# Kernel optimization log

Hardware: AMD Instinct MI355X
Metric: run time of the kernel (lower is better)

Reference implementation:

```python
import jax, jax.numpy as jnp
import numpy as np

K = 9
HF = WF = 128
SAMPLING = 16
H_IMG = W_IMG = 2048.0
ANC_RATIO = np.array([0.5, 1.0, 2.0])
ANC_SIZE = np.array([8.0, 16.0, 32.0])
TOPN_NMS = 6000
N_NMS = 2000
THR_NMS = 0.7


def generate_anchors():
    # loop order in original GenerateAnchor: ii over Wf (ctrx), jj over Hf (ctry), ratio, size
    ctrx = (np.arange(WF) + 0.5) * SAMPLING  # [Wf]
    ctry = (np.arange(HF) + 0.5) * SAMPLING  # [Hf]
    w = SAMPLING * ANC_SIZE[None, :] / np.sqrt(ANC_RATIO)[:, None]  # [R,S]
    h = SAMPLING * ANC_SIZE[None, :] * np.sqrt(ANC_RATIO)[:, None]
    cx = ctrx[:, None, None, None]  # [Wf,1,1,1]
    cy = ctry[None, :, None, None]  # [1,Hf,1,1]
    w = w[None, None]; h = h[None, None]  # [1,1,R,S]
    x1, y1 = cx - w / 2, cy - h / 2
    x2, y2 = cx + w / 2, cy + h / 2
    anc = np.stack(np.broadcast_arrays(x1, y1, x2, y2), axis=-1).reshape(-1, 4)
    return np.round(anc).astype(np.float32)  # [Wf*Hf*K, 4]


def conv2d(x, w, b, pad):
    y = jax.lax.conv_general_dilated(
        x, w, (1, 1), [(pad, pad), (pad, pad)],
        dimension_numbers=('NCHW', 'OIHW', 'NCHW'))
    return y + b[None, :, None, None]


def pairwise_iou(b):
    # Faithful to my_IoU: 'gt' (pivot, row i) coords are int-truncated;
    # intersection via min(all)+w_a+w_g-max(all); union uses raw/truncated areas.
    ax1, ay1, ax2, ay2 = b[:, 0], b[:, 1], b[:, 2], b[:, 3]
    aw, ah = ax2 - ax1, ay2 - ay1
    aminx, amaxx = jnp.minimum(ax1, ax2), jnp.maximum(ax1, ax2)
    aminy, amaxy = jnp.minimum(ay1, ay2), jnp.maximum(ay1, ay2)
    tx1, ty1, tx2, ty2 = jnp.trunc(ax1), jnp.trunc(ay1), jnp.trunc(ax2), jnp.trunc(ay2)
    gminx, gmaxx = jnp.minimum(tx1, tx2), jnp.maximum(tx1, tx2)
    gminy, gmaxy = jnp.minimum(ty1, ty2), jnp.maximum(ty1, ty2)
    gw, gh = jnp.trunc(ax2 - ax1), jnp.trunc(ay2 - ay1)
    iw = jnp.maximum(jnp.minimum(aminx[None, :], gminx[:, None]) + aw[None, :]
                     + gw[:, None] - jnp.maximum(amaxx[None, :], gmaxx[:, None]), 0.0)
    ih = jnp.maximum(jnp.minimum(aminy[None, :], gminy[:, None]) + ah[None, :]
                     + gh[:, None] - jnp.maximum(amaxy[None, :], gmaxy[:, None]), 0.0)
    inter = iw * ih  # [i=pivot, j=candidate]
    union = (aw * ah)[None, :] + (gw * gh)[:, None] - inter
    return inter / union


def make_roi(anchor, delta, obj):
    # delta2xy
    aw = anchor[:, 2] - anchor[:, 0]
    ah = anchor[:, 3] - anchor[:, 1]
    acx = anchor[:, 0] + aw / 2
    acy = anchor[:, 1] + ah / 2
    cx = delta[:, 0] * aw + acx
    cy = delta[:, 1] * ah + acy
    w = jnp.exp(delta[:, 2]) * aw
    h = jnp.exp(delta[:, 3]) * ah
    roi = jnp.stack([cx - w / 2, cy - h / 2, cx + w / 2, cy + h / 2], axis=1)
    # clip exactly as original: negatives->0; >H -> H-1; >W -> W-1
    roi = jnp.maximum(roi, 0.0)
    roi = roi.at[:, 3].set(jnp.where(roi[:, 3] > H_IMG, H_IMG - 1.0, roi[:, 3]))
    roi = roi.at[:, 2].set(jnp.where(roi[:, 2] > W_IMG, W_IMG - 1.0, roi[:, 2]))
    valid = (roi[:, 2] - roi[:, 0] > SAMPLING) & (roi[:, 3] - roi[:, 1] > SAMPLING)
    scores = jnp.where(valid, obj, -jnp.inf)  # mask instead of dropping (jit-friendly)
    top_scores, top_idx = jax.lax.top_k(scores, TOPN_NMS)
    boxes = roi[top_idx]
    keep0 = jnp.isfinite(top_scores)
    iou = pairwise_iou(boxes)  # [TOPN, TOPN]
    idxs = jnp.arange(TOPN_NMS)

    def body(i, keep):
        sup = keep[i] & (iou[i] >= THR_NMS) & (idxs > i)
        return keep & ~sup

    keep = jax.lax.fori_loop(0, TOPN_NMS, body, keep0)
    rank = jnp.cumsum(keep) - 1
    pos = jnp.where(keep & (rank < N_NMS), rank, N_NMS)  # out-of-range rows dropped
    out = jnp.zeros((N_NMS, 4), boxes.dtype).at[pos].set(boxes, mode='drop')
    return out


def setup_inputs() -> dict:
    key = jax.random.key(0)
    ks = jax.random.split(key, 4)
    featmap = jax.random.normal(ks[0], (1, 512, HF, WF), dtype=jnp.float32)
    conv3_w = jax.random.normal(ks[1], (512, 512, 3, 3), dtype=jnp.float32) * 0.01
    conv3_b = jnp.zeros((512,), jnp.float32)
    cls_w = jax.random.normal(ks[2], (2 * K, 512, 1, 1), dtype=jnp.float32) * 0.01
    cls_b = jnp.zeros((2 * K,), jnp.float32)
    reg_w = jax.random.normal(ks[3], (4 * K, 512, 1, 1), dtype=jnp.float32) * 0.01
    reg_b = jnp.zeros((4 * K,), jnp.float32)
    return {'featmap': featmap, 'conv3_w': conv3_w, 'conv3_b': conv3_b,
            'cls_w': cls_w, 'cls_b': cls_b, 'reg_w': reg_w, 'reg_b': reg_b}


def reference(featmap, conv3_w, conv3_b, cls_w, cls_b, reg_w, reg_b):
    x = jax.nn.relu(conv2d(featmap, conv3_w, conv3_b, 1))
    pred_cls = conv2d(x, cls_w, cls_b, 0)  # [1, 2k, Hf, Wf]
    pred_reg = conv2d(x, reg_w, reg_b, 0)  # [1, 4k, Hf, Wf]
    pred_cls = jnp.transpose(pred_cls, (0, 2, 3, 1)).reshape(1, -1, 2)
    pred_reg = jnp.transpose(pred_reg, (0, 2, 3, 1)).reshape(1, -1, 4)
    pred_obj = pred_cls[:, :, 1]
    anchors = jnp.asarray(generate_anchors())
    # roi path is detached in the original (uses .data)
    roi = make_roi(anchors,
                   jax.lax.stop_gradient(pred_reg[0]),
                   jax.lax.stop_gradient(pred_obj[0]))
    return roi, pred_cls, pred_reg
```

## Files before the change

kernel.cpp:

```cpp
#include <hip/hip_runtime.h>

#define HF 128
#define WF 128
#define KANC 9
#define NANC (HF*WF*KANC)
#define NSORT 262144
#define TOPN 6000
#define NWORDS 94
#define NOUT 2000
#define OFF_CLS 8000
#define OFF_REG 302912
#define NCAND 8192
#define NBCAP 2048

typedef unsigned long long u64;
typedef double d4 __attribute__((ext_vector_type(4)));
typedef const __attribute__((address_space(1))) void* gas1;
typedef __attribute__((address_space(3))) void* las3;

__global__ __launch_bounds__(256) void zero2_k(double* p1, int n1,
                                               double* p2, int n2) {
  int i = blockIdx.x * 256 + threadIdx.x;
  if (i < n1) p1[i] = 0.0;
  else if (i - n1 < n2) p2[i - n1] = 0.0;
}

__global__ __launch_bounds__(256) void wtrans_k(const float* __restrict__ w,
                                                float* __restrict__ wt) {
  __shared__ float ld[64 * 73];
  int t = threadIdx.x;
  int ocg = blockIdx.x & 7, icg = blockIdx.x >> 3;
  int oc0 = ocg << 6, ic0 = icg << 3;
  #pragma unroll
  for (int rep = 0; rep < 18; ++rep) {
    int idx = rep * 256 + t;
    int row = idx / 72, col = idx - row * 72;
    ld[row * 73 + col] = w[(size_t)(oc0 + row) * 4608 + ic0 * 9 + col];
  }
  __syncthreads();
  #pragma unroll
  for (int rep = 0; rep < 18; ++rep) {
    int idx = rep * 256 + t;
    int pair = idx >> 6, oc = idx & 63;
    int tap = pair % 9, ic = pair / 9;
    wt[(size_t)tap * 262144 + (size_t)(ic0 + ic) * 512 + oc0 + oc] =
        ld[oc * 73 + ic * 9 + tap];
  }
}

#define BKC 32
#define NCHUNK 144

__global__ __launch_bounds__(256, 3) void conv_mfma_k(
    const float* __restrict__ feat, const float* __restrict__ wt,
    const float* __restrict__ conv_b, const float* __restrict__ cls_w,
    const float* __restrict__ reg_w, double* __restrict__ predacc)
{
  __shared__ __align__(16) char smraw[49152];
  float* AsB = (float*)smraw;
  float* BsB = (float*)(smraw + 2 * 32 * 64 * 4);
  int tid = threadIdx.x;
  int bid = blockIdx.x;
  int pt = bid & 255, ot = bid >> 8;
  int h = pt >> 1, w0 = (pt & 1) << 6;
  int oc0 = ot << 7;
  int wv = tid >> 6, l = tid & 63;
  int wr = wv >> 1, wc = wv & 1;
  int lg = l >> 4, lr = l & 15;

  d4 acc[2][4];
  #pragma unroll
  for (int t = 0; t < 2; ++t)
    #pragma unroll
    for (int u = 0; u < 4; ++u) acc[t][u] = (d4)0.0;

  float4 areg[2];

  auto gloadA = [&](int c) {
    int tap = c >> 4, ic0 = (c & 15) << 5;
    int kh = tap / 3 - 1, kw = tap % 3 - 1;
    int hp = h + kh;
    bool okh = ((unsigned)hp < 128u);
    #pragma unroll
    for (int i = 0; i < 2; ++i) {
      int q = tid + (i << 8);
      int r = q >> 4, c0 = (q & 15) << 2;
      float v0 = 0.f, v1 = 0.f, v2 = 0.f, v3 = 0.f;
      const float* src = &feat[((ic0 + r) << 14) + (hp << 7)];
      int wp = w0 + c0 + kw;
      if (okh) {
        if ((unsigned)(wp + 0) < 128u) v0 = src[wp + 0];
        if ((unsigned)(wp + 1) < 128u) v1 = src[wp + 1];
        if ((unsigned)(wp + 2) < 128u) v2 = src[wp + 2];
        if ((unsigned)(wp + 3) < 128u) v3 = src[wp + 3];
      }
      areg[i] = make_float4(v0, v1, v2, v3);
    }
  };
  auto gloadB_lds = [&](int c, int buf) {
    float* B = BsB + buf * (32 * 128);
    #pragma unroll
    for (int i = 0; i < 4; ++i) {
      int q = tid + (i << 8);
      int r = q >> 5, c0 = (q & 31) << 2;
      const float* src =
          &wt[(size_t)((c << 5) + r) * 512 + oc0 + (c0 ^ ((r & 1) << 4))];
      __builtin_amdgcn_global_load_lds((gas1)src, (las3)&B[q << 2], 16, 0, 0);
    }
  };
  auto dswriteA = [&](int buf) {
    float* A = AsB + buf * (32 * 64);
    #pragma unroll
    for (int i = 0; i < 2; ++i) {
      int q = tid + (i << 8);
      int r = q >> 4, c0 = (q & 15) << 2;
      *(float4*)&A[(r << 6) + (c0 ^ ((r & 1) << 4))] = areg[i];
    }
  };
  auto compute = [&](int buf) {
    const float* A = AsB + buf * (32 * 64);
    const float* B = BsB + buf * (32 * 128);
    #pragma unroll
    for (int k4 = 0; k4 < BKC; k4 += 4) {
      int krow = k4 + lg;
      int sw = (krow & 1) << 4;
      double a0 = (double)A[(krow << 6) + (((wr << 5) + lr) ^ sw)];
      double a1 = (double)A[(krow << 6) + (((wr << 5) + 16 + lr) ^ sw)];
      double b0 = (double)B[(krow << 7) + (((wc << 6) + lr) ^ sw)];
      double b1 = (double)B[(krow << 7) + (((wc << 6) + 16 + lr) ^ sw)];
      double b2 = (double)B[(krow << 7) + (((wc << 6) + 32 + lr) ^ sw)];
      double b3 = (double)B[(krow << 7) + (((wc << 6) + 48 + lr) ^ sw)];
      acc[0][0] = __builtin_amdgcn_mfma_f64_16x16x4f64(a0, b0, acc[0][0], 0, 0, 0);
      acc[0][1] = __builtin_amdgcn_mfma_f64_16x16x4f64(a0, b1, acc[0][1], 0, 0, 0);
      acc[0][2] = __builtin_amdgcn_mfma_f64_16x16x4f64(a0, b2, acc[0][2], 0, 0, 0);
      acc[0][3] = __builtin_amdgcn_mfma_f64_16x16x4f64(a0, b3, acc[0][3], 0, 0, 0);
      acc[1][0] = __builtin_amdgcn_mfma_f64_16x16x4f64(a1, b0, acc[1][0], 0, 0, 0);
      acc[1][1] = __builtin_amdgcn_mfma_f64_16x16x4f64(a1, b1, acc[1][1], 0, 0, 0);
      acc[1][2] = __builtin_amdgcn_mfma_f64_16x16x4f64(a1, b2, acc[1][2], 0, 0, 0);
      acc[1][3] = __builtin_amdgcn_mfma_f64_16x16x4f64(a1, b3, acc[1][3], 0, 0, 0);
    }
  };

  gloadA(0);
  gloadB_lds(0, 0);
  dswriteA(0);
  for (int c = 0; c < NCHUNK; ++c) {
    __syncthreads();
    if (c + 1 < NCHUNK) {
      gloadB_lds(c + 1, (c + 1) & 1);
      gloadA(c + 1);
    }
    compute(c & 1);
    if (c + 1 < NCHUNK) dswriteA((c + 1) & 1);
  }

  int rmap[4], cmap[4];
  {
    d4 z = (d4)0.0;
    double apr = (lg == 0) ? (double)lr : 0.0;
    double bpr = (lg == 0) ? 1.0 : 0.0;
    d4 dr = __builtin_amdgcn_mfma_f64_16x16x4f64(apr, bpr, z, 0, 0, 0);
    double apc = (lg == 0) ? 1.0 : 0.0;
    double bpc = (lg == 0) ? (double)lr : 0.0;
    d4 dc = __builtin_amdgcn_mfma_f64_16x16x4f64(apc, bpc, z, 0, 0, 0);
    #pragma unroll
    for (int r = 0; r < 4; ++r) { rmap[r] = (int)dr[r]; cmap[r] = (int)dc[r]; }
  }

  double* xs = (double*)smraw;
  float* hwS = (float*)(smraw + 64 * 65 * 8);
  double sacc[14];
  #pragma unroll
  for (int it = 0; it < 14; ++it) sacc[it] = 0.0;

  #pragma unroll
  for (int hh = 0; hh < 2; ++hh) {
    __syncthreads();
    for (int e = tid; e < 54 * 64; e += 256) {
      int o = e >> 6, j = e & 63;
      int oc = oc0 + (hh << 6) + j;
      hwS[e] = (o < 18) ? cls_w[(o << 9) + oc] : reg_w[((o - 18) << 9) + oc];
    }
    if (wc == hh) {
      #pragma unroll
      for (int t = 0; t < 2; ++t) {
        #pragma unroll
        for (int u = 0; u < 4; ++u) {
          #pragma unroll
          for (int r = 0; r < 4; ++r) {
            int ocl = (u << 4) + cmap[r];
            int pxl = (wr << 5) + (t << 4) + rmap[r];
            double v = acc[t][u][r] + (double)conv_b[oc0 + (hh << 6) + ocl];
            xs[pxl * 65 + ocl] = (v > 0.0) ? v : 0.0;
          }
        }
      }
    }
    __syncthreads();
    #pragma unroll
    for (int it = 0; it < 14; ++it) {
      int e = tid + (it << 8);
      if (e < 54 * 64) {
        int o = e >> 6, px = e & 63;
        const double* xr = &xs[px * 65];
        const float* hr = &hwS[o << 6];
        double s = 0.0;
        #pragma unroll
        for (int j = 0; j < 64; ++j) s += xr[j] * (double)hr[j];
        sacc[it] += s;
      }
    }
  }
  int pixbase = (h << 7) + w0;
  #pragma unroll
  for (int it = 0; it < 14; ++it) {
    int e = tid + (it << 8);
    if (e < 54 * 64) {
      int o = e >> 6, px = e & 63;
      atomicAdd(&predacc[(size_t)(pixbase + px) * 54 + o], sacc[it]);
    }
  }
}

__global__ __launch_bounds__(256) void chk_x_k(
    const float* __restrict__ feat, const float* __restrict__ c3w,
    double* __restrict__ xraw)
{
  int task = blockIdx.x * 256 + threadIdx.x;
  int pi = task >> 12;
  int oc = (task >> 3) & 511;
  int icg = task & 7;
  const int pixs[4] = {0, 5437, 10240, 16383};
  int pix = pixs[pi];
  int h = pix >> 7, w = pix & 127;
  double s = 0.0;
  for (int ic = icg * 64; ic < icg * 64 + 64; ++ic) {
    const float* f = &feat[ic << 14];
    const float* wp = &c3w[(size_t)(oc * 512 + ic) * 9];
    #pragma unroll
    for (int kh = -1; kh <= 1; ++kh) {
      int hp = h + kh;
      if ((unsigned)hp >= 128u) continue;
      #pragma unroll
      for (int kw = -1; kw <= 1; ++kw) {
        int wq = w + kw;
        if ((unsigned)wq >= 128u) continue;
        s += (double)f[(hp << 7) + wq] * (double)wp[(kh + 1) * 3 + (kw + 1)];
      }
    }
  }
  atomicAdd(&xraw[(pi << 9) + oc], s);
}

__global__ __launch_bounds__(256) void chk_cmp_k(
    const double* __restrict__ xraw, const float* __restrict__ c3b,
    const float* __restrict__ cls_w, const float* __restrict__ reg_w,
    const double* __restrict__ predacc, double* flagd)
{
  int t = threadIdx.x;
  if (t >= 216) return;
  int pi = t / 54, o = t - pi * 54;
  const int pixs[4] = {0, 5437, 10240, 16383};
  const float* wrow = (o < 18) ? &cls_w[o << 9] : &reg_w[(o - 18) << 9];
  const double* xr = &xraw[pi << 9];
  double s = 0.0;
  for (int j = 0; j < 512; ++j) {
    double x = xr[j] + (double)c3b[j];
    x = x > 0.0 ? x : 0.0;
    s += x * (double)wrow[j];
  }
  double got = predacc[(size_t)pixs[pi] * 54 + o];
  if (fabs(got - s) > 1e-6) *flagd = 1.0;
}

__global__ __launch_bounds__(256) void rezero_k(const double* __restrict__ flagd,
                                                double* p, int n) {
  if (*flagd == 0.0) return;
  int i = blockIdx.x * 256 + threadIdx.x;
  if (i < n) p[i] = 0.0;
}

__global__ __launch_bounds__(256) void conv_fb_k(
    const double* __restrict__ flagd,
    const float* __restrict__ feat, const float* __restrict__ wt,
    const float* __restrict__ conv_b, const float* __restrict__ cls_w,
    const float* __restrict__ reg_w, double* __restrict__ predacc)
{
  if (*flagd == 0.0) return;
  __shared__ __align__(16) char smraw[47104];
  double* As = (double*)smraw;
  double* Bs = As + 2048;
  int tid = threadIdx.x;
  int bid = blockIdx.x;
  int pt = bid & 255, ot = bid >> 8;
  int h = pt >> 1, w0 = (pt & 1) << 6;
  int oc0 = ot << 6;
  int tx = tid & 15, ty = tid >> 4;

  double acc[4][4];
  #pragma unroll
  for (int i = 0; i < 4; ++i)
    #pragma unroll
    for (int j = 0; j < 4; ++j) acc[i][j] = 0.0;

  for (int tap = 0; tap < 9; ++tap) {
    int kh = tap / 3 - 1, kw = tap % 3 - 1;
    int hp = h + kh;
    bool okh = (hp >= 0) && (hp < HF);
    for (int icc = 0; icc < 16; ++icc) {
      int ic0 = icc << 5;
      __syncthreads();
      #pragma unroll
      for (int i = 0; i < 8; ++i) {
        int e = tid + (i << 8);
        int icl = e >> 6;
        int lx = e & 63;
        int wp = w0 + lx + kw;
        float v = 0.0f;
        if (okh && wp >= 0 && wp < WF)
          v = feat[((ic0 + icl) << 14) + (hp << 7) + wp];
        As[(icl << 6) + lx] = (double)v;
        Bs[(icl << 6) + lx] =
            (double)wt[((((tap << 9) + ic0 + icl)) << 9) + oc0 + lx];
      }
      __syncthreads();
      #pragma unroll
      for (int k = 0; k < 32; ++k) {
        const double* ar = &As[(k << 6) + (ty << 2)];
        const double* br = &Bs[(k << 6) + (tx << 2)];
        double a0 = ar[0], a1 = ar[1], a2 = ar[2], a3 = ar[3];
        double b0 = br[0], b1 = br[1], b2 = br[2], b3 = br[3];
        acc[0][0] += a0 * b0; acc[0][1] += a0 * b1; acc[0][2] += a0 * b2; acc[0][3] += a0 * b3;
        acc[1][0] += a1 * b0; acc[1][1] += a1 * b1; acc[1][2] += a1 * b2; acc[1][3] += a1 * b3;
        acc[2][0] += a2 * b0; acc[2][1] += a2 * b1; acc[2][2] += a2 * b2; acc[2][3] += a2 * b3;
        acc[3][0] += a3 * b0; acc[3][1] += a3 * b1; acc[3][2] += a3 * b2; acc[3][3] += a3 * b3;
      }
    }
  }
  __syncthreads();
  double* xs = (double*)smraw;
  float* hwS = (float*)(smraw + 64 * 65 * 8);
  #pragma unroll
  for (int i = 0; i < 4; ++i) {
    int px = (ty << 2) + i;
    #pragma unroll
    for (int j = 0; j < 4; ++j) {
      int oc = (tx << 2) + j;
      double v = acc[i][j] + (double)conv_b[oc0 + oc];
      xs[px * 65 + oc] = v > 0.0 ? v : 0.0;
    }
  }
  for (int e = tid; e < 54 * 64; e += 256) {
    int o = e >> 6, ocl = e & 63;
    hwS[e] = (o < 18) ? cls_w[(o << 9) + oc0 + ocl]
                      : reg_w[((o - 18) << 9) + oc0 + ocl];
  }
  __syncthreads();
  int pixbase = (h << 7) + w0;
  for (int e = tid; e < 54 * 64; e += 256) {
    int px = e & 63, o = e >> 6;
    const double* xr = &xs[px * 65];
    const float* hr = &hwS[o << 6];
    double s = 0.0;
    #pragma unroll
    for (int j = 0; j < 64; ++j) s += xr[j] * (double)hr[j];
    atomicAdd(&predacc[(pixbase + px) * 54 + o], s);
  }
}

__global__ __launch_bounds__(256) void anchor_k(
    const double* __restrict__ predacc, const float* __restrict__ cls_b,
    const float* __restrict__ reg_b, float* __restrict__ out,
    double* __restrict__ roi_all, double* __restrict__ scores_d,
    ulonglong2* __restrict__ sortb)
{
  #pragma clang fp contract(off)
  int a = blockIdx.x * 256 + threadIdx.x;
  if (a >= NSORT) return;
  if (a >= NANC) {
    sortb[a] = make_ulonglong2(0xFFF0000000000000ULL, 0xFFFFFFFFULL);
    return;
  }
  int pix = a / 9;
  int k = a - pix * 9;
  int h = pix >> 7, wq = pix & 127;
  const double* pa = &predacc[pix * 54];
  double c0 = pa[2 * k] + (double)cls_b[2 * k];
  double c1 = pa[2 * k + 1] + (double)cls_b[2 * k + 1];
  double d0 = pa[18 + 4 * k + 0] + (double)reg_b[4 * k + 0];
  double d1 = pa[18 + 4 * k + 1] + (double)reg_b[4 * k + 1];
  double d2 = pa[18 + 4 * k + 2] + (double)reg_b[4 * k + 2];
  double d3 = pa[18 + 4 * k + 3] + (double)reg_b[4 * k + 3];
  out[OFF_CLS + a * 2 + 0] = (float)c0;
  out[OFF_CLS + a * 2 + 1] = (float)c1;
  out[OFF_REG + a * 4 + 0] = (float)d0;
  out[OFF_REG + a * 4 + 1] = (float)d1;
  out[OFF_REG + a * 4 + 2] = (float)d2;
  out[OFF_REG + a * 4 + 3] = (float)d3;
  int ir = k / 3, is = k - ir * 3;
  double ratio = (ir == 0) ? 0.5 : (ir == 1 ? 1.0 : 2.0);
  double asz = (is == 0) ? 8.0 : (is == 1 ? 16.0 : 32.0);
  double sq = sqrt(ratio);
  double wa = (16.0 * asz) / sq;
  double ha = (16.0 * asz) * sq;
  double cx = (h + 0.5) * 16.0;
  double cy = (wq + 0.5) * 16.0;
  double A0 = (double)(float)rint(cx - wa * 0.5);
  double A1 = (double)(float)rint(cy - ha * 0.5);
  double A2 = (double)(float)rint(cx + wa * 0.5);
  double A3 = (double)(float)rint(cy + ha * 0.5);
  double aw = A2 - A0, ah = A3 - A1;
  double acx = A0 + aw * 0.5, acy = A1 + ah * 0.5;
  double ccx = d0 * aw + acx;
  double ccy = d1 * ah + acy;
  double wr = exp(d2) * aw;
  double hh = exp(d3) * ah;
  double r0 = ccx - wr * 0.5;
  double r1 = ccy - hh * 0.5;
  double r2 = ccx + wr * 0.5;
  double r3 = ccy + hh * 0.5;
  r0 = fmax(r0, 0.0); r1 = fmax(r1, 0.0); r2 = fmax(r2, 0.0); r3 = fmax(r3, 0.0);
  r3 = (r3 > 2048.0) ? 2047.0 : r3;
  r2 = (r2 > 2048.0) ? 2047.0 : r2;
  bool valid = ((r2 - r0) > 16.0) && ((r3 - r1) > 16.0);
  double score = valid ? c1 : -__builtin_huge_val();
  roi_all[a * 4 + 0] = r0;
  roi_all[a * 4 + 1] = r1;
  roi_all[a * 4 + 2] = r2;
  roi_all[a * 4 + 3] = r3;
  scores_d[a] = score;
  u64 u = (u64)__double_as_longlong(score);
  u64 m = (u >> 63) ? ~u : (u | 0x8000000000000000ULL);
  sortb[a] = make_ulonglong2(~m, (u64)a);
}

__global__ __launch_bounds__(1024) void init_sel_k(unsigned* hist, u64* selp,
                                                   unsigned* cnt) {
  int t = blockIdx.x * 1024 + threadIdx.x;
  if (t < 2048) hist[t] = 0;
  if (t == 0) { selp[0] = 0; selp[1] = 0; cnt[0] = 0; cnt[1] = 0; }
}

__global__ __launch_bounds__(1024) void hist_k(const ulonglong2* __restrict__ sortb,
                                               unsigned* __restrict__ hist,
                                               const u64* __restrict__ selp,
                                               int pass) {
  __shared__ unsigned h[2048];
  int t = threadIdx.x;
  h[t] = 0; h[t + 1024] = 0;
  __syncthreads();
  const int SH[3] = {53, 42, 31};
  const u64 PM[3] = {0ULL, 0xFFE0000000000000ULL, 0xFFFFFC0000000000ULL};
  u64 pfx = selp[0];
  u64 pm = PM[pass];
  int sh = SH[pass];
  for (int e = blockIdx.x * 1024 + t; e < NSORT; e += gridDim.x * 1024) {
    u64 k = sortb[e].x;
    if ((k & pm) == pfx)
      atomicAdd(&h[(unsigned)((k >> sh) & 2047)], 1u);
  }
  __syncthreads();
  if (h[t]) atomicAdd(&hist[t], h[t]);
  if (h[t + 1024]) atomicAdd(&hist[t + 1024], h[t + 1024]);
}

__global__ __launch_bounds__(1024) void scan_k(unsigned* hist, u64* selp, int pass) {
  __shared__ unsigned h[2048];
  int t = threadIdx.x;
  h[t] = hist[t]; h[t + 1024] = hist[t + 1024];
  hist[t] = 0; hist[t + 1024] = 0;
  __syncthreads();
  if (t == 0) {
    const int SH[3] = {53, 42, 31};
    u64 cum = selp[1];
    u64 pfx = selp[0];
    int b = 0;
    for (; b < 2047; ++b) {
      if (cum + h[b] >= (u64)TOPN) break;
      cum += h[b];
    }
    selp[0] = pfx | ((u64)b << SH[pass]);
    selp[1] = cum;
  }
}

__global__ __launch_bounds__(1024) void compact_k(
    const ulonglong2* __restrict__ sortb, const u64* __restrict__ selp,
    ulonglong2* __restrict__ cand, ulonglong2* __restrict__ bcand,
    unsigned* __restrict__ cnt) {
  u64 pfx = selp[0];
  const u64 M33 = 0xFFFFFFFF80000000ULL;
  for (int e = blockIdx.x * 1024 + threadIdx.x; e < NSORT; e += gridDim.x * 1024) {
    ulonglong2 v = sortb[e];
    u64 top = v.x & M33;
    if (top < pfx) {
      unsigned p = atomicAdd(&cnt[0], 1u);
      if (p < NCAND) cand[p] = v;
    } else if (top == pfx) {
      unsigned p = atomicAdd(&cnt[1], 1u);
      if (p < NBCAP) bcand[p] = v;
    }
  }
}

__global__ __launch_bounds__(1024) void fill_k(ulonglong2* cand,
                                               const ulonglong2* __restrict__ bcand,
                                               const unsigned* __restrict__ cnt) {
  int t = blockIdx.x * 1024 + threadIdx.x;
  unsigned ci = cnt[0];
  unsigned cb = cnt[1] < NBCAP ? cnt[1] : NBCAP;
  if (t >= (int)ci) {
    if (t < (int)(ci + cb)) cand[t] = bcand[t - ci];
    else if (t < NCAND) cand[t] = make_ulonglong2(~0ULL, ~0ULL);
  }
}

__device__ __forceinline__ bool sless(ulonglong2 A, ulonglong2 B) {
  return (A.x < B.x) || (A.x == B.x && A.y < B.y);
}

__global__ __launch_bounds__(1024) void sort8k_k(ulonglong2* d) {
  extern __shared__ ulonglong2 s[];
  int t = threadIdx.x;
  #pragma unroll
  for (int i = 0; i < 8; ++i) s[t + (i << 10)] = d[t + (i << 10)];
  __syncthreads();
  for (int k = 2; k <= NCAND; k <<= 1) {
    for (int j = k >> 1; j >= 1; j >>= 1) {
      #pragma unroll
      for (int q = 0; q < 4; ++q) {
        int p = t + (q << 10);
        int li = ((p & ~(j - 1)) << 1) | (p & (j - 1));
        int pa = li | j;
        bool asc = ((li & k) == 0);
        ulonglong2 A = s[li], B = s[pa];
        bool sw = asc ? sless(B, A) : sless(A, B);
        if (sw) { s[li] = B; s[pa] = A; }
      }
      __syncthreads();
    }
  }
  #pragma unroll
  for (int i = 0; i < 8; ++i) d[t + (i << 10)] = s[t + (i << 10)];
}

__global__ __launch_bounds__(1024) void prep_k(
    const ulonglong2* __restrict__ sorted, const double* __restrict__ roi_all,
    const double* __restrict__ scores_d, double* __restrict__ boxes,
    u64* __restrict__ removed)
{
  int t = threadIdx.x;
  for (int i = t; i < TOPN; i += 1024) {
    unsigned idx = (unsigned)sorted[i].y;
    double b0 = 0, b1 = 0, b2 = 0, b3 = 0;
    if (idx < NANC) {
      b0 = roi_all[idx * 4 + 0];
      b1 = roi_all[idx * 4 + 1];
      b2 = roi_all[idx * 4 + 2];
      b3 = roi_all[idx * 4 + 3];
    }
    boxes[i * 4 + 0] = b0; boxes[i * 4 + 1] = b1;
    boxes[i * 4 + 2] = b2; boxes[i * 4 + 3] = b3;
  }
  if (t < NWORDS) {
    u64 wdd = (t == NWORDS - 1) ? 0xFFFF000000000000ULL : 0ULL;
    for (int b = 0; b < 64; ++b) {
      int i = t * 64 + b;
      if (i >= TOPN) break;
      unsigned idx = (unsigned)sorted[i].y;
      bool dead = true;
      if (idx < NANC) dead = isinf(scores_d[idx]);
      if (dead) wdd |= (1ULL << b);
    }
    removed[t] = wdd;
  }
}

__global__ __launch_bounds__(256) void mask_k(const double* __restrict__ boxes,
                                              u64* __restrict__ mask) {
  #pragma clang fp contract(off)
  int gw = (blockIdx.x * 256 + threadIdx.x) >> 6;
  int lane = threadIdx.x & 63;
  int i = gw / NWORDS, wj = gw - i * NWORDS;
  if (i >= TOPN) return;
  if (wj < (i >> 6)) return;
  double ix1 = boxes[i * 4 + 0], iy1 = boxes[i * 4 + 1];
  double ix2 = boxes[i * 4 + 2], iy2 = boxes[i * 4 + 3];
  double tx1 = trunc(ix1), ty1 = trunc(iy1), tx2 = trunc(ix2), ty2 = trunc(iy2);
  double gminx = fmin(tx1, tx2), gmaxx = fmax(tx1, tx2);
  double gminy = fmin(ty1, ty2), gmaxy = fmax(ty1, ty2);
  double gw_ = trunc(ix2 - ix1), gh_ = trunc(iy2 - iy1);
  int j = wj * 64 + lane;
  bool pred = false;
  if (j < TOPN && j > i) {
    double jx1 = boxes[j * 4 + 0], jy1 = boxes[j * 4 + 1];
    double jx2 = boxes[j * 4 + 2], jy2 = boxes[j * 4 + 3];
    double aw = jx2 - jx1, ah = jy2 - jy1;
    double aminx = fmin(jx1, jx2), amaxx = fmax(jx1, jx2);
    double aminy = fmin(jy1, jy2), amaxy = fmax(jy1, jy2);
    double iw = fmin(aminx, gminx) + aw + gw_ - fmax(amaxx, gmaxx);
    iw = fmax(iw, 0.0);
    double ih = fmin(aminy, gminy) + ah + gh_ - fmax(amaxy, gmaxy);
    ih = fmax(ih, 0.0);
    double inter = iw * ih;
    double uni = aw * ah + gw_ * gh_ - inter;
    pred = (inter / uni >= 0.7);
  }
  u64 bal = __ballot(pred);
  if (lane == 0) mask[(size_t)i * NWORDS + wj] = bal;
}

__global__ __launch_bounds__(1024) void nms_chunk_k(const u64* __restrict__ mask,
                                                    u64* removed_g) {
  __shared__ u64 rem[NWORDS];
  __shared__ u64 aliveSh;
  int t = threadIdx.x;
  int lane = t & 63;
  int wvid = t >> 6;
  if (t < NWORDS) rem[t] = removed_g[t];
  __syncthreads();
  for (int c = 0; c < NWORDS; ++c) {
    if (wvid == 0) {
      int i = c * 64 + lane;
      u64 diag = (i < TOPN) ? mask[(size_t)i * NWORDS + c] : 0ULL;
      u64 local = rem[c];
      #pragma unroll 1
      for (int j = 0; j < 64; ++j) {
        u64 dj = __shfl(diag, j);
        if (!((local >> j) & 1ULL)) local |= dj;
      }
      if (lane == 0) { rem[c] = local; aliveSh = ~local; }
    }
    __syncthreads();
    u64 alive = aliveSh;
    int nw = NWORDS - 1 - c;
    if (nw > 0 && alive) {
      int npairs = 64 * nw;
      for (int p = t; p < npairs; p += 1024) {
        int j = p / nw;
        int w = c + 1 + (p - j * nw);
        if ((alive >> j) & 1ULL) {
          int i = c * 64 + j;
          if (i < TOPN) {
            u64 v = mask[(size_t)i * NWORDS + w];
            if (v) atomicOr(&rem[w], v);
          }
        }
      }
    }
    __syncthreads();
  }
  if (t < NWORDS) removed_g[t] = rem[t];
}

__global__ __launch_bounds__(256) void out_k(const u64* __restrict__ removed,
                                             const double* __restrict__ boxes,
                                             float* __restrict__ out) {
  __shared__ int pref[NWORDS + 1];
  __shared__ u64 keepw[NWORDS];
  int t = threadIdx.x;
  for (int i = t; i < NOUT * 4; i += 256) out[i] = 0.0f;
  if (t < NWORDS) keepw[t] = ~removed[t];
  __syncthreads();
  if (t == 0) {
    int s = 0;
    for (int w = 0; w < NWORDS; ++w) { pref[w] = s; s += __popcll(keepw[w]); }
    pref[NWORDS] = s;
  }
  __syncthreads();
  for (int i = t; i < TOPN; i += 256) {
    u64 kw = keepw[i >> 6];
    if ((kw >> (i & 63)) & 1ULL) {
      int rank = pref[i >> 6] + __popcll(kw & ((1ULL << (i & 63)) - 1ULL));
      if (rank < NOUT) {
        out[rank * 4 + 0] = (float)boxes[i * 4 + 0];
        out[rank * 4 + 1] = (float)boxes[i * 4 + 1];
        out[rank * 4 + 2] = (float)boxes[i * 4 + 2];
        out[rank * 4 + 3] = (float)boxes[i * 4 + 3];
      }
    }
  }
}

extern "C" void kernel_launch(void* const* d_in, const int* in_sizes, int n_in,
                              void* d_out, int out_size, void* d_ws, size_t ws_size,
                              hipStream_t stream) {
  const float* feat = (const float*)d_in[0];
  const float* c3w = (const float*)d_in[1];
  const float* c3b = (const float*)d_in[2];
  const float* clw = (const float*)d_in[3];
  const float* clb = (const float*)d_in[4];
  const float* rgw = (const float*)d_in[5];
  const float* rgb = (const float*)d_in[6];
  float* out = (float*)d_out;
  char* ws = (char*)d_ws;
  size_t off = 0;
  auto alloc = [&](size_t bytes) {
    size_t o = off;
    off = (off + bytes + 255) & ~(size_t)255;
    return o;
  };
  double* predacc = (double*)(ws + alloc(16384ULL * 54 * 8));
  double* flagd = (double*)(ws + alloc(256));
  float* wt = (float*)(ws + alloc(2359296ULL * 4));
  double* roi_all = (double*)(ws + alloc((size_t)NANC * 4 * 8));
  double* scores_d = (double*)(ws + alloc((size_t)NANC * 8));
  ulonglong2* sortb = (ulonglong2*)(ws + alloc((size_t)NSORT * 16));
  double* boxes = (double*)(ws + alloc((size_t)TOPN * 4 * 8));
  u64* mask = (u64*)(ws + alloc((size_t)TOPN * NWORDS * 8));
  u64* removed = (u64*)(ws + alloc(NWORDS * 8));
  double* xraw = (double*)(ws + alloc(4 * 512 * 8));
  unsigned* hist = (unsigned*)(ws + alloc(2048 * 4));
  u64* selp = (u64*)(ws + alloc(256));
  unsigned* cntb = (unsigned*)(ws + alloc(256));
  ulonglong2* cand = (ulonglong2*)(ws + alloc((size_t)NCAND * 16));
  ulonglong2* bcand = (ulonglong2*)(ws + alloc((size_t)NBCAP * 16));
  (void)ws_size; (void)out_size; (void)in_sizes; (void)n_in;

  const int NPRED = 16384 * 54;
  hipLaunchKernelGGL(zero2_k, dim3((NPRED + 32 + 2048 + 255) / 256), dim3(256), 0,
                     stream, predacc, NPRED + 32, xraw, 2048);
  hipLaunchKernelGGL(wtrans_k, dim3(512), dim3(256), 0, stream, c3w, wt);
  hipLaunchKernelGGL(conv_mfma_k, dim3(1024), dim3(256), 0, stream,
                     feat, wt, c3b, clw, rgw, predacc);
  hipLaunchKernelGGL(chk_x_k, dim3(64), dim3(256), 0, stream, feat, c3w, xraw);
  hipLaunchKernelGGL(chk_cmp_k, dim3(1), dim3(256), 0, stream,
                     xraw, c3b, clw, rgw, predacc, flagd);
  hipLaunchKernelGGL(rezero_k, dim3((NPRED + 255) / 256), dim3(256), 0, stream,
                     flagd, predacc, NPRED);
  hipLaunchKernelGGL(conv_fb_k, dim3(2048), dim3(256), 0, stream,
                     flagd, feat, wt, c3b, clw, rgw, predacc);
  hipLaunchKernelGGL(anchor_k, dim3(NSORT / 256), dim3(256), 0, stream,
                     predacc, clb, rgb, out, roi_all, scores_d, sortb);
  hipLaunchKernelGGL(init_sel_k, dim3(2), dim3(1024), 0, stream, hist, selp, cntb);
  for (int pass = 0; pass < 3; ++pass) {
    hipLaunchKernelGGL(hist_k, dim3(128), dim3(1024), 0, stream,
                       sortb, hist, selp, pass);
    hipLaunchKernelGGL(scan_k, dim3(1), dim3(1024), 0, stream, hist, selp, pass);
  }
  hipLaunchKernelGGL(compact_k, dim3(128), dim3(1024), 0, stream,
                     sortb, selp, cand, bcand, cntb);
  hipLaunchKernelGGL(fill_k, dim3(NCAND / 1024), dim3(1024), 0, stream,
                     cand, bcand, cntb);
  hipLaunchKernelGGL(sort8k_k, dim3(1), dim3(1024), NCAND * 16, stream, cand);
  hipLaunchKernelGGL(prep_k, dim3(1), dim3(1024), 0, stream,
                     cand, roi_all, scores_d, boxes, removed);
  hipLaunchKernelGGL(mask_k, dim3(TOPN * NWORDS / 4), dim3(256), 0, stream,
                     boxes, mask);
  hipLaunchKernelGGL(nms_chunk_k, dim3(1), dim3(1024), 0, stream, mask, removed);
  hipLaunchKernelGGL(out_k, dim3(1), dim3(256), 0, stream, removed, boxes, out);
}
```

Baseline: 2.519 ms.

## Shrink conv output-channel tile to 64, fuse small selection and sort kernels

```diff
diff --git a/kernel.cpp b/kernel.cpp
--- a/kernel.cpp
+++ b/kernel.cpp
@@ -18,11 +18,15 @@
 typedef const __attribute__((address_space(1))) void* gas1;
 typedef __attribute__((address_space(3))) void* las3;
 
-__global__ __launch_bounds__(256) void zero2_k(double* p1, int n1,
-                                               double* p2, int n2) {
+__global__ __launch_bounds__(256) void zero3_k(double* p1, int n1,
+                                               double* p2, int n2,
+                                               unsigned* hist, u64* selp,
+                                               unsigned* cnt) {
   int i = blockIdx.x * 256 + threadIdx.x;
   if (i < n1) p1[i] = 0.0;
   else if (i - n1 < n2) p2[i - n1] = 0.0;
+  if (i < 2048) hist[i] = 0;
+  if (i == 0) { selp[0] = 0; selp[1] = 0; cnt[0] = 0; cnt[1] = 0; }
 }
 
 __global__ __launch_bounds__(256) void wtrans_k(const float* __restrict__ w,
@@ -51,28 +55,28 @@
 #define BKC 32
 #define NCHUNK 144
 
-__global__ __launch_bounds__(256, 3) void conv_mfma_k(
+__global__ __launch_bounds__(256, 4) void conv_mfma_k(
     const float* __restrict__ feat, const float* __restrict__ wt,
     const float* __restrict__ conv_b, const float* __restrict__ cls_w,
     const float* __restrict__ reg_w, double* __restrict__ predacc)
 {
-  __shared__ __align__(16) char smraw[49152];
+  __shared__ __align__(16) char smraw[32768];
   float* AsB = (float*)smraw;
-  float* BsB = (float*)(smraw + 2 * 32 * 64 * 4);
+  float* BsB = (float*)(smraw + 2 * 2048 * 4);
   int tid = threadIdx.x;
   int bid = blockIdx.x;
   int pt = bid & 255, ot = bid >> 8;
   int h = pt >> 1, w0 = (pt & 1) << 6;
-  int oc0 = ot << 7;
+  int oc0 = ot << 6;
   int wv = tid >> 6, l = tid & 63;
   int wr = wv >> 1, wc = wv & 1;
   int lg = l >> 4, lr = l & 15;
 
-  d4 acc[2][4];
+  d4 acc[2][2];
   #pragma unroll
   for (int t = 0; t < 2; ++t)
     #pragma unroll
-    for (int u = 0; u < 4; ++u) acc[t][u] = (d4)0.0;
+    for (int u = 0; u < 2; ++u) acc[t][u] = (d4)0.0;
 
   float4 areg[2];
 
@@ -98,18 +102,18 @@
     }
   };
   auto gloadB_lds = [&](int c, int buf) {
-    float* B = BsB + buf * (32 * 128);
-    #pragma unroll
-    for (int i = 0; i < 4; ++i) {
+    float* B = BsB + buf * 2048;
+    #pragma unroll
+    for (int i = 0; i < 2; ++i) {
       int q = tid + (i << 8);
-      int r = q >> 5, c0 = (q & 31) << 2;
+      int r = q >> 4, c0 = (q & 15) << 2;
       const float* src =
           &wt[(size_t)((c << 5) + r) * 512 + oc0 + (c0 ^ ((r & 1) << 4))];
       __builtin_amdgcn_global_load_lds((gas1)src, (las3)&B[q << 2], 16, 0, 0);
     }
   };
   auto dswriteA = [&](int buf) {
-    float* A = AsB + buf * (32 * 64);
+    float* A = AsB + buf * 2048;
     #pragma unroll
     for (int i = 0; i < 2; ++i) {
       int q = tid + (i << 8);
@@ -118,26 +122,20 @@
     }
   };
   auto compute = [&](int buf) {
-    const float* A = AsB + buf * (32 * 64);
-    const float* B = BsB + buf * (32 * 128);
+    const float* A = AsB + buf * 2048;
+    const float* B = BsB + buf * 2048;
     #pragma unroll
     for (int k4 = 0; k4 < BKC; k4 += 4) {
       int krow = k4 + lg;
       int sw = (krow & 1) << 4;
       double a0 = (double)A[(krow << 6) + (((wr << 5) + lr) ^ sw)];
       double a1 = (double)A[(krow << 6) + (((wr << 5) + 16 + lr) ^ sw)];
-      double b0 = (double)B[(krow << 7) + (((wc << 6) + lr) ^ sw)];
-      double b1 = (double)B[(krow << 7) + (((wc << 6) + 16 + lr) ^ sw)];
-      double b2 = (double)B[(krow << 7) + (((wc << 6) + 32 + lr) ^ sw)];
-      double b3 = (double)B[(krow << 7) + (((wc << 6) + 48 + lr) ^ sw)];
+      double b0 = (double)B[(krow << 6) + (((wc << 5) + lr) ^ sw)];
+      double b1 = (double)B[(krow << 6) + (((wc << 5) + 16 + lr) ^ sw)];
       acc[0][0] = __builtin_amdgcn_mfma_f64_16x16x4f64(a0, b0, acc[0][0], 0, 0, 0);
       acc[0][1] = __builtin_amdgcn_mfma_f64_16x16x4f64(a0, b1, acc[0][1], 0, 0, 0);
-      acc[0][2] = __builtin_amdgcn_mfma_f64_16x16x4f64(a0, b2, acc[0][2], 0, 0, 0);
-      acc[0][3] = __builtin_amdgcn_mfma_f64_16x16x4f64(a0, b3, acc[0][3], 0, 0, 0);
       acc[1][0] = __builtin_amdgcn_mfma_f64_16x16x4f64(a1, b0, acc[1][0], 0, 0, 0);
       acc[1][1] = __builtin_amdgcn_mfma_f64_16x16x4f64(a1, b1, acc[1][1], 0, 0, 0);
-      acc[1][2] = __builtin_amdgcn_mfma_f64_16x16x4f64(a1, b2, acc[1][2], 0, 0, 0);
-      acc[1][3] = __builtin_amdgcn_mfma_f64_16x16x4f64(a1, b3, acc[1][3], 0, 0, 0);
     }
   };
 
@@ -168,29 +166,26 @@
   }
 
   double* xs = (double*)smraw;
-  float* hwS = (float*)(smraw + 64 * 65 * 8);
-  double sacc[14];
+  float* hwS = (float*)(smraw + 32 * 65 * 8);
+  __syncthreads();
+  for (int e = tid; e < 54 * 64; e += 256) {
+    int o = e >> 6, j = e & 63;
+    hwS[e] = (o < 18) ? cls_w[(o << 9) + oc0 + j]
+                      : reg_w[((o - 18) << 9) + oc0 + j];
+  }
+  int pixbase = (h << 7) + w0;
   #pragma unroll
-  for (int it = 0; it < 14; ++it) sacc[it] = 0.0;
-
-  #pragma unroll
-  for (int hh = 0; hh < 2; ++hh) {
-    __syncthreads();
-    for (int e = tid; e < 54 * 64; e += 256) {
-      int o = e >> 6, j = e & 63;
-      int oc = oc0 + (hh << 6) + j;
-      hwS[e] = (o < 18) ? cls_w[(o << 9) + oc] : reg_w[((o - 18) << 9) + oc];
-    }
-    if (wc == hh) {
+  for (int ph = 0; ph < 2; ++ph) {
+    if (wr == ph) {
       #pragma unroll
       for (int t = 0; t < 2; ++t) {
         #pragma unroll
-        for (int u = 0; u < 4; ++u) {
+        for (int u = 0; u < 2; ++u) {
           #pragma unroll
           for (int r = 0; r < 4; ++r) {
-            int ocl = (u << 4) + cmap[r];
-            int pxl = (wr << 5) + (t << 4) + rmap[r];
-            double v = acc[t][u][r] + (double)conv_b[oc0 + (hh << 6) + ocl];
+            int ocl = (wc << 5) + (u << 4) + cmap[r];
+            int pxl = (t << 4) + rmap[r];
+            double v = acc[t][u][r] + (double)conv_b[oc0 + ocl];
             xs[pxl * 65 + ocl] = (v > 0.0) ? v : 0.0;
           }
         }
@@ -198,27 +193,19 @@
     }
     __syncthreads();
     #pragma unroll
-    for (int it = 0; it < 14; ++it) {
+    for (int it = 0; it < 7; ++it) {
       int e = tid + (it << 8);
-      if (e < 54 * 64) {
-        int o = e >> 6, px = e & 63;
+      if (e < 54 * 32) {
+        int o = e >> 5, px = e & 31;
         const double* xr = &xs[px * 65];
         const float* hr = &hwS[o << 6];
         double s = 0.0;
         #pragma unroll
         for (int j = 0; j < 64; ++j) s += xr[j] * (double)hr[j];
-        sacc[it] += s;
-      }
-    }
-  }
-  int pixbase = (h << 7) + w0;
-  #pragma unroll
-  for (int it = 0; it < 14; ++it) {
-    int e = tid + (it << 8);
-    if (e < 54 * 64) {
-      int o = e >> 6, px = e & 63;
-      atomicAdd(&predacc[(size_t)(pixbase + px) * 54 + o], sacc[it]);
-    }
+        atomicAdd(&predacc[(size_t)(pixbase + (ph << 5) + px) * 54 + o], s);
+      }
+    }
+    __syncthreads();
   }
 }
 
@@ -227,14 +214,14 @@
     double* __restrict__ xraw)
 {
   int task = blockIdx.x * 256 + threadIdx.x;
-  int pi = task >> 12;
-  int oc = (task >> 3) & 511;
-  int icg = task & 7;
+  int pi = task >> 14;
+  int oc = (task >> 5) & 511;
+  int icg = task & 31;
   const int pixs[4] = {0, 5437, 10240, 16383};
   int pix = pixs[pi];
   int h = pix >> 7, w = pix & 127;
   double s = 0.0;
-  for (int ic = icg * 64; ic < icg * 64 + 64; ++ic) {
+  for (int ic = icg * 16; ic < icg * 16 + 16; ++ic) {
     const float* f = &feat[ic << 14];
     const float* wp = &c3w[(size_t)(oc * 512 + ic) * 9];
     #pragma unroll
@@ -434,13 +421,6 @@
   sortb[a] = make_ulonglong2(~m, (u64)a);
 }
 
-__global__ __launch_bounds__(1024) void init_sel_k(unsigned* hist, u64* selp,
-                                                   unsigned* cnt) {
-  int t = blockIdx.x * 1024 + threadIdx.x;
-  if (t < 2048) hist[t] = 0;
-  if (t == 0) { selp[0] = 0; selp[1] = 0; cnt[0] = 0; cnt[1] = 0; }
-}
-
 __global__ __launch_bounds__(1024) void hist_k(const ulonglong2* __restrict__ sortb,
                                                unsigned* __restrict__ hist,
                                                const u64* __restrict__ selp,
@@ -503,27 +483,29 @@
   }
 }
 
-__global__ __launch_bounds__(1024) void fill_k(ulonglong2* cand,
-                                               const ulonglong2* __restrict__ bcand,
-                                               const unsigned* __restrict__ cnt) {
-  int t = blockIdx.x * 1024 + threadIdx.x;
-  unsigned ci = cnt[0];
-  unsigned cb = cnt[1] < NBCAP ? cnt[1] : NBCAP;
-  if (t >= (int)ci) {
-    if (t < (int)(ci + cb)) cand[t] = bcand[t - ci];
-    else if (t < NCAND) cand[t] = make_ulonglong2(~0ULL, ~0ULL);
-  }
-}
-
 __device__ __forceinline__ bool sless(ulonglong2 A, ulonglong2 B) {
   return (A.x < B.x) || (A.x == B.x && A.y < B.y);
 }
 
-__global__ __launch_bounds__(1024) void sort8k_k(ulonglong2* d) {
+__global__ __launch_bounds__(1024) void sortprep_k(
+    const ulonglong2* __restrict__ cand, const ulonglong2* __restrict__ bcand,
+    const unsigned* __restrict__ cnt, const double* __restrict__ roi_all,
+    const double* __restrict__ scores_d, double* __restrict__ boxes,
+    u64* __restrict__ removed)
+{
   extern __shared__ ulonglong2 s[];
   int t = threadIdx.x;
+  unsigned ci = cnt[0]; if (ci > NCAND) ci = NCAND;
+  unsigned cb = cnt[1]; if (cb > NBCAP) cb = NBCAP;
   #pragma unroll
-  for (int i = 0; i < 8; ++i) s[t + (i << 10)] = d[t + (i << 10)];
+  for (int i = 0; i < 8; ++i) {
+    int p = t + (i << 10);
+    ulonglong2 v;
+    if (p < (int)ci) v = cand[p];
+    else if (p < (int)(ci + cb)) v = bcand[p - ci];
+    else v = make_ulonglong2(~0ULL, ~0ULL);
+    s[p] = v;
+  }
   __syncthreads();
   for (int k = 2; k <= NCAND; k <<= 1) {
     for (int j = k >> 1; j >= 1; j >>= 1) {
@@ -540,18 +522,8 @@
       __syncthreads();
     }
   }
-  #pragma unroll
-  for (int i = 0; i < 8; ++i) d[t + (i << 10)] = s[t + (i << 10)];
-}
-
-__global__ __launch_bounds__(1024) void prep_k(
-    const ulonglong2* __restrict__ sorted, const double* __restrict__ roi_all,
-    const double* __restrict__ scores_d, double* __restrict__ boxes,
-    u64* __restrict__ removed)
-{
-  int t = threadIdx.x;
   for (int i = t; i < TOPN; i += 1024) {
-    unsigned idx = (unsigned)sorted[i].y;
+    unsigned idx = (unsigned)s[i].y;
     double b0 = 0, b1 = 0, b2 = 0, b3 = 0;
     if (idx < NANC) {
       b0 = roi_all[idx * 4 + 0];
@@ -567,7 +539,7 @@
     for (int b = 0; b < 64; ++b) {
       int i = t * 64 + b;
       if (i >= TOPN) break;
-      unsigned idx = (unsigned)sorted[i].y;
+      unsigned idx = (unsigned)s[i].y;
       bool dead = true;
       if (idx < NANC) dead = isinf(scores_d[idx]);
       if (dead) wdd |= (1ULL << b);
@@ -718,12 +690,12 @@
   (void)ws_size; (void)out_size; (void)in_sizes; (void)n_in;
 
   const int NPRED = 16384 * 54;
-  hipLaunchKernelGGL(zero2_k, dim3((NPRED + 32 + 2048 + 255) / 256), dim3(256), 0,
-                     stream, predacc, NPRED + 32, xraw, 2048);
+  hipLaunchKernelGGL(zero3_k, dim3((NPRED + 32 + 2048 + 255) / 256), dim3(256), 0,
+                     stream, predacc, NPRED + 32, xraw, 2048, hist, selp, cntb);
   hipLaunchKernelGGL(wtrans_k, dim3(512), dim3(256), 0, stream, c3w, wt);
-  hipLaunchKernelGGL(conv_mfma_k, dim3(1024), dim3(256), 0, stream,
+  hipLaunchKernelGGL(conv_mfma_k, dim3(2048), dim3(256), 0, stream,
                      feat, wt, c3b, clw, rgw, predacc);
-  hipLaunchKernelGGL(chk_x_k, dim3(64), dim3(256), 0, stream, feat, c3w, xraw);
+  hipLaunchKernelGGL(chk_x_k, dim3(256), dim3(256), 0, stream, feat, c3w, xraw);
   hipLaunchKernelGGL(chk_cmp_k, dim3(1), dim3(256), 0, stream,
                      xraw, c3b, clw, rgw, predacc, flagd);
   hipLaunchKernelGGL(rezero_k, dim3((NPRED + 255) / 256), dim3(256), 0, stream,
@@ -732,7 +704,6 @@
                      flagd, feat, wt, c3b, clw, rgw, predacc);
   hipLaunchKernelGGL(anchor_k, dim3(NSORT / 256), dim3(256), 0, stream,
                      predacc, clb, rgb, out, roi_all, scores_d, sortb);
-  hipLaunchKernelGGL(init_sel_k, dim3(2), dim3(1024), 0, stream, hist, selp, cntb);
   for (int pass = 0; pass < 3; ++pass) {
     hipLaunchKernelGGL(hist_k, dim3(128), dim3(1024), 0, stream,
                        sortb, hist, selp, pass);
@@ -740,11 +711,8 @@
   }
   hipLaunchKernelGGL(compact_k, dim3(128), dim3(1024), 0, stream,
                      sortb, selp, cand, bcand, cntb);
-  hipLaunchKernelGGL(fill_k, dim3(NCAND / 1024), dim3(1024), 0, stream,
-                     cand, bcand, cntb);
-  hipLaunchKernelGGL(sort8k_k, dim3(1), dim3(1024), NCAND * 16, stream, cand);
-  hipLaunchKernelGGL(prep_k, dim3(1), dim3(1024), 0, stream,
-                     cand, roi_all, scores_d, boxes, removed);
+  hipLaunchKernelGGL(sortprep_k, dim3(1), dim3(1024), NCAND * 16, stream,
+                     cand, bcand, cntb, roi_all, scores_d, boxes, removed);
   hipLaunchKernelGGL(mask_k, dim3(TOPN * NWORDS / 4), dim3(256), 0, stream,
                      boxes, mask);
   hipLaunchKernelGGL(nms_chunk_k, dim3(1), dim3(1024), 0, stream, mask, removed);
```

Result: faster. 2.379 ms (-5.6%).
